# Kernel optimization log

Measured on AMD Instinct MI355X. Metric: run time of the kernel, lower is better.

Reference implementation:

```python
import jax, jax.numpy as jnp
import numpy as np

DIM = 768
N_HEADS = 12
HEAD_DIM = DIM // N_HEADS
MAX_REL = 3  # hardcoded in the module


def setup_inputs() -> dict:
    key = jax.random.key(0)
    ks = jax.random.split(key, 10)
    B, L = 4, 1024
    def xavier(k, shape):
        fan_in, fan_out = shape[-2], shape[-1]
        a = jnp.sqrt(6.0 / (fan_in + fan_out))
        return jax.random.uniform(k, shape, jnp.float32, -a, a)
    return {
        "query": jax.random.normal(ks[0], (B, L, DIM), jnp.float32),
        "key":   jax.random.normal(ks[1], (B, L, DIM), jnp.float32),
        "value": jax.random.normal(ks[2], (B, L, DIM), jnp.float32),
        "Wq": xavier(ks[3], (DIM, DIM)),
        "Wk": xavier(ks[4], (DIM, DIM)),
        "Wv": xavier(ks[5], (DIM, DIM)),
        "Wproj": xavier(ks[6], (DIM, DIM)),
        "b_proj": jnp.zeros((DIM,), jnp.float32),
        "rel_k_table": xavier(ks[7], (2 * MAX_REL + 1, HEAD_DIM)),
        "rel_v_table": xavier(ks[8], (2 * MAX_REL + 1, HEAD_DIM)),
    }


def _rel_embed(table, len_q, len_k):
    # [len_q, len_k, head_dim] gathered from clipped relative distances
    dist = jnp.arange(len_k)[None, :] - jnp.arange(len_q)[:, None]
    idx = jnp.clip(dist, -MAX_REL, MAX_REL) + MAX_REL
    return table[idx]


def reference(query, key, value, Wq, Wk, Wv, Wproj, b_proj, rel_k_table, rel_v_table):
    B, Lq, _ = query.shape
    Lk = key.shape[1]
    H, hd = N_HEADS, HEAD_DIM
    scale = hd ** (-0.5)

    q = query @ Wq.T                      # [B, Lq, D]
    k = key @ Wk.T                        # [B, Lk, D]
    v = value @ Wv.T                      # [B, Lk, D]

    qh = q.reshape(B, Lq, H, hd).transpose(0, 2, 1, 3)   # [B,H,Lq,hd]
    kh = k.reshape(B, Lk, H, hd).transpose(0, 2, 1, 3)
    vh = v.reshape(B, Lk, H, hd).transpose(0, 2, 1, 3)

    # content-content scores
    attn1 = jnp.einsum('bhqd,bhkd->bhqk', qh, kh)
    # content-relative-position scores
    rk = _rel_embed(rel_k_table, Lq, Lk)                  # [Lq,Lk,hd]
    attn2 = jnp.einsum('bhqd,qkd->bhqk', qh, rk)
    # NOTE: original code DIVIDES by scale (= hd**-0.5), i.e. multiplies by sqrt(hd)
    attn = (attn1 + attn2) / scale
    attn = jax.nn.softmax(attn, axis=-1)                  # [B,H,Lq,Lk]

    w1 = jnp.einsum('bhqk,bhkd->bhqd', attn, vh)
    rv = _rel_embed(rel_v_table, Lq, Lk)                  # [Lq,Lk,hd]
    w2 = jnp.einsum('bhqk,qkd->bhqd', attn, rv)

    x = (w1 + w2).transpose(0, 2, 1, 3).reshape(B, Lq, H * hd)
    x = x @ Wproj.T + b_proj
    return (x, attn)
```

## Files before the change

### kernel.cpp

```cpp
#include <hip/hip_runtime.h>

#define DIMM 768
#define NH 12
#define HD 64
#define LSEQ 1024
#define BATCH 4
#define NXE 3145728
#define NWE 589824

typedef __bf16 bf16x8 __attribute__((ext_vector_type(8)));
typedef float f32x4 __attribute__((ext_vector_type(4)));
typedef unsigned short u16;

static __device__ __forceinline__ u16 f2bf(float f) {
  unsigned u = __builtin_bit_cast(unsigned, f);
  u += 0x7fffu + ((u >> 16) & 1u);
  return (u16)(u >> 16);
}
static __device__ __forceinline__ float bf2f(u16 h) {
  unsigned u = ((unsigned)h) << 16;
  return __builtin_bit_cast(float, u);
}
static __device__ __forceinline__ bf16x8 ld8bf(const u16* p) {
  uint4 u = *(const uint4*)p;
  return __builtin_bit_cast(bf16x8, u);
}
#define MFMA(a, b, c) __builtin_amdgcn_mfma_f32_16x16x32_bf16(a, b, c, 0, 0, 0)
#define LGKM0_FENCE()                                      \
  do {                                                     \
    asm volatile("s_waitcnt lgkmcnt(0)" ::: "memory");     \
    __builtin_amdgcn_sched_barrier(0);                     \
    __builtin_amdgcn_s_barrier();                          \
  } while (0)

__global__ __launch_bounds__(256) void convert(
    const float* __restrict__ q_in, const float* __restrict__ k_in,
    const float* __restrict__ v_in, const float* __restrict__ Wq,
    const float* __restrict__ Wk, const float* __restrict__ Wv,
    const float* __restrict__ Wp, u16* __restrict__ AqH, u16* __restrict__ AqL,
    u16* __restrict__ AkH, u16* __restrict__ AkL, u16* __restrict__ Av,
    u16* __restrict__ WqH, u16* __restrict__ WqL, u16* __restrict__ WkH,
    u16* __restrict__ WkL, u16* __restrict__ Wvr, u16* __restrict__ Wpr) {
  long i = ((long)blockIdx.x * 256 + threadIdx.x) * 4;
  const float* src;
  u16 *dh, *dl = nullptr;
  long off;
  if (i < NXE) { src = q_in; dh = AqH; dl = AqL; off = i; }
  else if (i < 2L * NXE) { src = k_in; dh = AkH; dl = AkL; off = i - NXE; }
  else if (i < 3L * NXE) { src = v_in; dh = Av; off = i - 2L * NXE; }
  else {
    long j = i - 3L * NXE;
    int which = (int)(j / NWE);
    off = j % NWE;
    if (which == 0) { src = Wq; dh = WqH; dl = WqL; }
    else if (which == 1) { src = Wk; dh = WkH; dl = WkL; }
    else if (which == 2) { src = Wv; dh = Wvr; }
    else { src = Wp; dh = Wpr; }
  }
  float4 v = *(const float4*)(src + off);
  ushort4 h;
  h.x = f2bf(v.x); h.y = f2bf(v.y); h.z = f2bf(v.z); h.w = f2bf(v.w);
  *(ushort4*)(dh + off) = h;
  if (dl) {
    ushort4 lo;
    lo.x = f2bf(v.x - bf2f(h.x)); lo.y = f2bf(v.y - bf2f(h.y));
    lo.z = f2bf(v.z - bf2f(h.z)); lo.w = f2bf(v.w - bf2f(h.w));
    *(ushort4*)(dl + off) = lo;
  }
}

__device__ __forceinline__ void gemm_body(
    int mode, const u16* AqH, const u16* AqL, const u16* AkH, const u16* AkL,
    const u16* Av, const u16* WqH, const u16* WqL, const u16* WkH,
    const u16* WkL, const u16* Wvr, const u16* Wpr, const u16* wbuf,
    u16* qhi, u16* qlo, u16* khi, u16* klo, u16* vT, float* outp,
    const float* bias) {
  __shared__ u16 sAh[2][64 * 32], sAl[2][64 * 32];
  __shared__ u16 sBh[2][128 * 32], sBl[2][128 * 32];
  const u16 *Ah, *Al = nullptr, *Bh, *Bl = nullptr;
  if (mode == 0) { Ah = AqH; Al = AqL; Bh = WqH; Bl = WqL; }
  else if (mode == 1) { Ah = AkH; Al = AkL; Bh = WkH; Bl = WkL; }
  else if (mode == 2) { Ah = Av; Bh = Wvr; }
  else { Ah = wbuf; Bh = Wpr; }
  const int t = threadIdx.x, w = t >> 6, l = t & 63;
  const int quad = l >> 4, l15 = l & 15;
  const int flat = blockIdx.x + 64 * blockIdx.y;
  const int swz = (flat & 7) * 48 + (flat >> 3);
  const int m0 = (swz & 63) * 64, n0 = (swz >> 6) * 128;
  const int wm = (w & 1) * 32, wn = (w >> 1) * 64;
  const int srow = t >> 2, scol = (t & 3) * 8;
  const int t8 = t * 8;
  const u16* gA = Ah + (m0 + srow) * DIMM + scol;
  const u16* gB = Bh + (n0 + srow) * DIMM + scol;
  const u16* gAl = (mode < 2) ? Al + (m0 + srow) * DIMM + scol : nullptr;
  const u16* gBl = (mode < 2) ? Bl + (n0 + srow) * DIMM + scol : nullptr;
  f32x4 acc[2][4] = {};
  uint4 rA, rB0, rB1, rAl, rBl0, rBl1;

  if (mode < 2) {
#define LOADS2(k0n)                                                  \
    do {                                                             \
      rA = *(const uint4*)(gA + (k0n));                              \
      rB0 = *(const uint4*)(gB + (k0n));                             \
      rB1 = *(const uint4*)(gB + 64 * DIMM + (k0n));                 \
      rAl = *(const uint4*)(gAl + (k0n));                            \
      rBl0 = *(const uint4*)(gBl + (k0n));                           \
      rBl1 = *(const uint4*)(gBl + 64 * DIMM + (k0n));               \
    } while (0)
#define DSW2(p)                                                      \
    do {                                                             \
      *(uint4*)(&sAh[p][t8]) = rA;                                   \
      *(uint4*)(&sBh[p][t8]) = rB0;                                  \
      *(uint4*)(&sBh[p][t8 + 2048]) = rB1;                           \
      *(uint4*)(&sAl[p][t8]) = rAl;                                  \
      *(uint4*)(&sBl[p][t8]) = rBl0;                                 \
      *(uint4*)(&sBl[p][t8 + 2048]) = rBl1;                          \
    } while (0)
#define FRAGS2(p)                                                    \
    do {                                                             \
      _Pragma("unroll") for (int i = 0; i < 2; ++i) {                \
        ah[i] = __builtin_bit_cast(bf16x8,                           \
            *(const uint4*)(&sAh[p][(wm + i * 16 + l15) * 32 + quad * 8])); \
        al[i] = __builtin_bit_cast(bf16x8,                           \
            *(const uint4*)(&sAl[p][(wm + i * 16 + l15) * 32 + quad * 8])); \
      }                                                              \
      _Pragma("unroll") for (int j = 0; j < 4; ++j) {                \
        bh[j] = __builtin_bit_cast(bf16x8,                           \
            *(const uint4*)(&sBh[p][(wn + j * 16 + l15) * 32 + quad * 8])); \
        bl[j] = __builtin_bit_cast(bf16x8,                           \
            *(const uint4*)(&sBl[p][(wn + j * 16 + l15) * 32 + quad * 8])); \
      }                                                              \
    } while (0)
#define MFMAS2()                                                     \
    do {                                                             \
      _Pragma("unroll") for (int i = 0; i < 2; ++i)                  \
        _Pragma("unroll") for (int j = 0; j < 4; ++j)                \
          acc[i][j] = MFMA(ah[i], bh[j], acc[i][j]);                 \
      _Pragma("unroll") for (int i = 0; i < 2; ++i)                  \
        _Pragma("unroll") for (int j = 0; j < 4; ++j)                \
          acc[i][j] = MFMA(al[i], bh[j], acc[i][j]);                 \
      _Pragma("unroll") for (int i = 0; i < 2; ++i)                  \
        _Pragma("unroll") for (int j = 0; j < 4; ++j)                \
          acc[i][j] = MFMA(ah[i], bl[j], acc[i][j]);                 \
    } while (0)
    LOADS2(0);
    DSW2(0);
    LOADS2(32);
    LGKM0_FENCE();
    for (int k0 = 0; k0 < DIMM; k0 += 64) {
      bf16x8 ah[2], al[2], bh[4], bl[4];
      FRAGS2(0);
      DSW2(1);
      if (k0 + 64 < DIMM) LOADS2(k0 + 64);
      MFMAS2();
      LGKM0_FENCE();
      FRAGS2(1);
      if (k0 + 64 < DIMM) {
        DSW2(0);
        if (k0 + 96 < DIMM) LOADS2(k0 + 96);
      }
      MFMAS2();
      if (k0 + 64 < DIMM) LGKM0_FENCE();
    }
#undef LOADS2
#undef DSW2
#undef FRAGS2
#undef MFMAS2
  } else {
#define LOADS1(k0n)                                                  \
    do {                                                             \
      rA = *(const uint4*)(gA + (k0n));                              \
      rB0 = *(const uint4*)(gB + (k0n));                             \
      rB1 = *(const uint4*)(gB + 64 * DIMM + (k0n));                 \
    } while (0)
#define DSW1(p)                                                      \
    do {                                                             \
      *(uint4*)(&sAh[p][t8]) = rA;                                   \
      *(uint4*)(&sBh[p][t8]) = rB0;                                  \
      *(uint4*)(&sBh[p][t8 + 2048]) = rB1;                           \
    } while (0)
#define FRAGS1(p)                                                    \
    do {                                                             \
      _Pragma("unroll") for (int i = 0; i < 2; ++i)                  \
        ah[i] = __builtin_bit_cast(bf16x8,                           \
            *(const uint4*)(&sAh[p][(wm + i * 16 + l15) * 32 + quad * 8])); \
      _Pragma("unroll") for (int j = 0; j < 4; ++j)                  \
        bh[j] = __builtin_bit_cast(bf16x8,                           \
            *(const uint4*)(&sBh[p][(wn + j * 16 + l15) * 32 + quad * 8])); \
    } while (0)
#define MFMAS1()                                                     \
    do {                                                             \
      _Pragma("unroll") for (int i = 0; i < 2; ++i)                  \
        _Pragma("unroll") for (int j = 0; j < 4; ++j)                \
          acc[i][j] = MFMA(ah[i], bh[j], acc[i][j]);                 \
    } while (0)
    LOADS1(0);
    DSW1(0);
    LOADS1(32);
    LGKM0_FENCE();
    for (int k0 = 0; k0 < DIMM; k0 += 64) {
      bf16x8 ah[2], bh[4];
      FRAGS1(0);
      DSW1(1);
      if (k0 + 64 < DIMM) LOADS1(k0 + 64);
      MFMAS1();
      LGKM0_FENCE();
      FRAGS1(1);
      if (k0 + 64 < DIMM) {
        DSW1(0);
        if (k0 + 96 < DIMM) LOADS1(k0 + 96);
      }
      MFMAS1();
      if (k0 + 64 < DIMM) LGKM0_FENCE();
    }
#undef LOADS1
#undef DSW1
#undef FRAGS1
#undef MFMAS1
  }

  u16* oh = (mode == 0) ? qhi : khi;
  u16* ol = (mode == 0) ? qlo : klo;
#pragma unroll
  for (int i = 0; i < 2; ++i)
#pragma unroll
    for (int j = 0; j < 4; ++j)
#pragma unroll
      for (int r = 0; r < 4; ++r) {
        int grow = m0 + wm + i * 16 + quad * 4 + r;
        int gcol = n0 + wn + j * 16 + l15;
        float c = acc[i][j][r];
        int b = grow >> 10, ll = grow & 1023, h = gcol >> 6, d = gcol & 63;
        if (mode < 2) {
          int idx = ((b * NH + h) * LSEQ + ll) * HD + d;
          u16 hi = f2bf(c);
          oh[idx] = hi;
          ol[idx] = f2bf(c - bf2f(hi));
        } else if (mode == 2) {
          vT[((b * NH + h) * HD + d) * LSEQ + ll] = f2bf(c);
        } else {
          outp[grow * DIMM + gcol] = c + bias[gcol];
        }
      }
}

__global__ __launch_bounds__(256, 3) void gemm_qkv(
    const u16* __restrict__ AqH, const u16* __restrict__ AqL,
    const u16* __restrict__ AkH, const u16* __restrict__ AkL,
    const u16* __restrict__ Av, const u16* __restrict__ WqH,
    const u16* __restrict__ WqL, const u16* __restrict__ WkH,
    const u16* __restrict__ WkL, const u16* __restrict__ Wvr,
    const u16* __restrict__ Wpr, const u16* __restrict__ wbuf,
    u16* __restrict__ qhi, u16* __restrict__ qlo, u16* __restrict__ khi,
    u16* __restrict__ klo, u16* __restrict__ vT, float* __restrict__ outp,
    const float* __restrict__ bias) {
  gemm_body(blockIdx.z, AqH, AqL, AkH, AkL, Av, WqH, WqL, WkH, WkL, Wvr, Wpr,
            wbuf, qhi, qlo, khi, klo, vT, outp, bias);
}

__global__ __launch_bounds__(256, 3) void gemm_proj(
    const u16* __restrict__ AqH, const u16* __restrict__ AqL,
    const u16* __restrict__ AkH, const u16* __restrict__ AkL,
    const u16* __restrict__ Av, const u16* __restrict__ WqH,
    const u16* __restrict__ WqL, const u16* __restrict__ WkH,
    const u16* __restrict__ WkL, const u16* __restrict__ Wvr,
    const u16* __restrict__ Wpr, const u16* __restrict__ wbuf,
    u16* __restrict__ qhi, u16* __restrict__ qlo, u16* __restrict__ khi,
    u16* __restrict__ klo, u16* __restrict__ vT, float* __restrict__ outp,
    const float* __restrict__ bias) {
  gemm_body(3, AqH, AqL, AkH, AkL, Av, WqH, WqL, WkH, WkL, Wvr, Wpr,
            wbuf, qhi, qlo, khi, klo, vT, outp, bias);
}

__global__ __launch_bounds__(256, 3) void attn_core(
    const u16* __restrict__ qhi, const u16* __restrict__ qlo,
    const u16* __restrict__ khi, const u16* __restrict__ klo,
    const u16* __restrict__ vT, const float* __restrict__ relk,
    const float* __restrict__ relv, float* __restrict__ attn_out,
    u16* __restrict__ wbuf) {
  __shared__ __align__(16) u16 uni[16 * 1032];
  __shared__ float qrel[16][7];
  __shared__ float arel[16][7];
  __shared__ float rvt[7][64];
  __shared__ float red[4][16][4];

  const int Lb = blockIdx.x + 64 * (blockIdx.y + NH * blockIdx.z);
  const int flat = (Lb & 7) * 384 + (Lb >> 3);
  const int qt = flat & 63, h = (flat >> 6) % NH, b = flat / (64 * NH);
  const int q0 = qt * 16;
  const int tid = threadIdx.x, wave = tid >> 6, lane = tid & 63;
  const int quad = lane >> 4, l15 = lane & 15;
  const int bhd = b * NH + h;

  const int rs = tid >> 3;
  const int cg = (tid & 7) ^ (rs & 7);
  const u16* gh = khi + (bhd * LSEQ + rs) * HD + cg * 8;
  const u16* gl = klo + (bhd * LSEQ + rs) * HD + cg * 8;
  u16* const wslot = uni + tid * 8;
  const int rowA = wave * 16 + l15;
  const int sw = rowA & 7;
  const int s0 = (rowA * 8 + (quad ^ sw)) * 8;
  const int s1 = (rowA * 8 + ((quad + 4) ^ sw)) * 8;

  uint4 sA0, sA1, sA2, sA3, sB0, sB1, sB2, sB3;
#define LOADA(c)                                                     \
  do {                                                               \
    sA0 = *(const uint4*)(gh + (c) * (64 * HD));                     \
    sA1 = *(const uint4*)(gh + (c) * (64 * HD) + 32 * HD);           \
    sA2 = *(const uint4*)(gl + (c) * (64 * HD));                     \
    sA3 = *(const uint4*)(gl + (c) * (64 * HD) + 32 * HD);           \
  } while (0)
#define LOADB(c)                                                     \
  do {                                                               \
    sB0 = *(const uint4*)(gh + (c) * (64 * HD));                     \
    sB1 = *(const uint4*)(gh + (c) * (64 * HD) + 32 * HD);           \
    sB2 = *(const uint4*)(gl + (c) * (64 * HD));                     \
    sB3 = *(const uint4*)(gl + (c) * (64 * HD) + 32 * HD);           \
  } while (0)
#define DSWRITE_A(bufsel)                                            \
  do {                                                               \
    u16* d_ = wslot + (bufsel) * 8192;                               \
    *(uint4*)(d_) = sA0;                                             \
    *(uint4*)(d_ + 2048) = sA1;                                      \
    *(uint4*)(d_ + 4096) = sA2;                                      \
    *(uint4*)(d_ + 6144) = sA3;                                      \
  } while (0)
#define DSWRITE_B(bufsel)                                            \
  do {                                                               \
    u16* d_ = wslot + (bufsel) * 8192;                               \
    *(uint4*)(d_) = sB0;                                             \
    *(uint4*)(d_ + 2048) = sB1;                                      \
    *(uint4*)(d_ + 4096) = sB2;                                      \
    *(uint4*)(d_ + 6144) = sB3;                                      \
  } while (0)

  const int qbase = (bhd * LSEQ + q0 + l15) * HD + quad * 8;
  bf16x8 ah0 = ld8bf(qhi + qbase);
  bf16x8 ah1 = ld8bf(qhi + qbase + 32);
  bf16x8 al0 = ld8bf(qlo + qbase);
  bf16x8 al1 = ld8bf(qlo + qbase + 32);
  LOADA(0);
  LOADB(1);

  for (int t = tid; t < 7 * HD; t += 256) rvt[t >> 6][t & 63] = relv[t];
  if (tid < 112) {
    int q = tid / 7, rr = tid % 7;
    const u16* qp = qhi + (bhd * LSEQ + q0 + q) * HD;
    const u16* lp = qlo + (bhd * LSEQ + q0 + q) * HD;
    const float* tp = relk + rr * HD;
    float s = 0.f;
#pragma unroll
    for (int d8 = 0; d8 < HD; d8 += 8) {
      uint4 uh = *(const uint4*)(qp + d8);
      uint4 ul = *(const uint4*)(lp + d8);
      float4 t0 = *(const float4*)(tp + d8);
      float4 t1 = *(const float4*)(tp + d8 + 4);
      unsigned hh[4] = {uh.x, uh.y, uh.z, uh.w};
      unsigned lv[4] = {ul.x, ul.y, ul.z, ul.w};
      float tv[8] = {t0.x, t0.y, t0.z, t0.w, t1.x, t1.y, t1.z, t1.w};
#pragma unroll
      for (int m = 0; m < 4; ++m) {
        s += (bf2f((u16)(hh[m] & 0xffff)) + bf2f((u16)(lv[m] & 0xffff))) * tv[2 * m];
        s += (bf2f((u16)(hh[m] >> 16)) + bf2f((u16)(lv[m] >> 16))) * tv[2 * m + 1];
      }
    }
    qrel[q][rr] = s;
    arel[q][rr] = 0.f;
  }

  DSWRITE_A(0);
  asm volatile("s_waitcnt lgkmcnt(0)" ::: "memory");
  __builtin_amdgcn_sched_barrier(0);
  __builtin_amdgcn_s_barrier();

  f32x4 sc[16];
#pragma unroll
  for (int c = 0; c < 16; ++c) {
    const u16* cur = uni + (c & 1) * 8192;
    bf16x8 kh0 = ld8bf(cur + s0);
    bf16x8 kh1 = ld8bf(cur + s1);
    bf16x8 kl0 = ld8bf(cur + 4096 + s0);
    bf16x8 kl1 = ld8bf(cur + 4096 + s1);
    f32x4 e = {}, f = {};
    e = MFMA(ah0, kh0, e);
    f = MFMA(ah1, kh1, f);
    e = MFMA(ah0, kl0, e);
    f = MFMA(ah1, kl1, f);
    e = MFMA(al0, kh0, e);
    f = MFMA(al1, kh1, f);
    sc[c] = e + f;
    if (c < 14) {
      if ((c & 1) == 0) LOADA(c + 2); else LOADB(c + 2);
    }
    if (c < 15) {
      if ((c & 1) == 0) DSWRITE_B(1); else DSWRITE_A(0);
      asm volatile("s_waitcnt lgkmcnt(0)" ::: "memory");
      __builtin_amdgcn_sched_barrier(0);
      __builtin_amdgcn_s_barrier();
    }
  }
#undef LOADA
#undef LOADB
#undef DSWRITE_A
#undef DSWRITE_B

  const int colbase = wave * 16 + l15;
  const int dbase = colbase - q0 - quad * 4;
  float mrow[4] = {-3.4e38f, -3.4e38f, -3.4e38f, -3.4e38f};
#pragma unroll
  for (int c = 0; c < 16; ++c)
#pragma unroll
    for (int r = 0; r < 4; ++r) {
      int d = dbase + c * 64 - r;
      int ri = d < -3 ? 0 : (d > 3 ? 6 : d + 3);
      float s = (sc[c][r] + qrel[quad * 4 + r][ri]) * 8.0f;
      sc[c][r] = s;
      mrow[r] = fmaxf(mrow[r], s);
    }
#pragma unroll
  for (int m = 1; m <= 8; m <<= 1)
#pragma unroll
    for (int r = 0; r < 4; ++r) mrow[r] = fmaxf(mrow[r], __shfl_xor(mrow[r], m));
  if (l15 < 4) {
    float mv = l15 == 0 ? mrow[0] : l15 == 1 ? mrow[1] : l15 == 2 ? mrow[2] : mrow[3];
    red[0][quad * 4 + l15][wave] = mv;
  }
  __syncthreads();
  float mx[4];
#pragma unroll
  for (int r = 0; r < 4; ++r) {
    int row = quad * 4 + r;
    mx[r] = fmaxf(fmaxf(red[0][row][0], red[0][row][1]),
                  fmaxf(red[0][row][2], red[0][row][3]));
  }

  float sum[4] = {}, s0a[4] = {}, s6a[4] = {};
#pragma unroll
  for (int c = 0; c < 16; ++c)
#pragma unroll
    for (int r = 0; r < 4; ++r) {
      float e = __expf(sc[c][r] - mx[r]);
      sc[c][r] = e;
      int d = dbase + c * 64 - r;
      sum[r] += e;
      if (d <= -3) s0a[r] += e;
      if (d >= 3) s6a[r] += e;
    }
#pragma unroll
  for (int m = 1; m <= 8; m <<= 1)
#pragma unroll
    for (int r = 0; r < 4; ++r) {
      sum[r] += __shfl_xor(sum[r], m);
      s0a[r] += __shfl_xor(s0a[r], m);
      s6a[r] += __shfl_xor(s6a[r], m);
    }
  if (l15 < 4) {
    int row = quad * 4 + l15;
    float sv = l15 == 0 ? sum[0] : l15 == 1 ? sum[1] : l15 == 2 ? sum[2] : sum[3];
    float a0 = l15 == 0 ? s0a[0] : l15 == 1 ? s0a[1] : l15 == 2 ? s0a[2] : s0a[3];
    float a6 = l15 == 0 ? s6a[0] : l15 == 1 ? s6a[1] : l15 == 2 ? s6a[2] : s6a[3];
    red[1][row][wave] = sv;
    red[2][row][wave] = a0;
    red[3][row][wave] = a6;
  }
  __syncthreads();
  float rn[4];
#pragma unroll
  for (int r = 0; r < 4; ++r) {
    int row = quad * 4 + r;
    float s = red[1][row][0] + red[1][row][1] + red[1][row][2] + red[1][row][3];
    rn[r] = 1.0f / s;
    if (wave == 0 && l15 == 0) {
      float t0 = red[2][row][0] + red[2][row][1] + red[2][row][2] + red[2][row][3];
      float t6 = red[3][row][0] + red[3][row][1] + red[3][row][2] + red[3][row][3];
      arel[row][0] = t0 * rn[r];
      arel[row][6] = t6 * rn[r];
    }
  }

#pragma unroll
  for (int c = 0; c < 16; ++c) {
    int col = colbase + c * 64;
#pragma unroll
    for (int r = 0; r < 4; ++r) {
      int row = quad * 4 + r;
      float p = sc[c][r] * rn[r];
      uni[row * 1032 + col] = f2bf(p);
      int d = dbase + c * 64 - r;
      if (d >= -2 && d <= 2) arel[row][d + 3] = p;
    }
  }
  __syncthreads();

  {
    float* aob = attn_out + ((size_t)(bhd * LSEQ + q0)) * LSEQ;
#pragma unroll
    for (int row = 0; row < 16; ++row) {
      uint2 u = *(const uint2*)&uni[row * 1032 + tid * 4];
      float4 f = {bf2f((u16)(u.x & 0xffff)), bf2f((u16)(u.x >> 16)),
                  bf2f((u16)(u.y & 0xffff)), bf2f((u16)(u.y >> 16))};
      *(float4*)(aob + row * LSEQ + tid * 4) = f;
    }
  }

  {
    const u16* vb = vT + (bhd * HD + wave * 16 + l15) * LSEQ;
    f32x4 acc0 = {}, acc1 = {};
#pragma unroll 4
    for (int kk = 0; kk < LSEQ; kk += 64) {
      int ak = kk + quad * 8;
      bf16x8 aP0 = __builtin_bit_cast(bf16x8, *(const uint4*)&uni[l15 * 1032 + ak]);
      bf16x8 bV0 = ld8bf(vb + ak);
      acc0 = MFMA(aP0, bV0, acc0);
      bf16x8 aP1 = __builtin_bit_cast(bf16x8, *(const uint4*)&uni[l15 * 1032 + ak + 32]);
      bf16x8 bV1 = ld8bf(vb + ak + 32);
      acc1 = MFMA(aP1, bV1, acc1);
    }
    f32x4 acc = acc0 + acc1;
    const int col = wave * 16 + l15;
#pragma unroll
    for (int r = 0; r < 4; ++r) {
      int row = quad * 4 + r;
      float w2 = 0.f;
#pragma unroll
      for (int t = 0; t < 7; ++t) w2 += arel[row][t] * rvt[t][col];
      wbuf[(b * LSEQ + q0 + row) * DIMM + h * HD + col] = f2bf(acc[r] + w2);
    }
  }
}

extern "C" void kernel_launch(void* const* d_in, const int* in_sizes, int n_in,
                              void* d_out, int out_size, void* d_ws, size_t ws_size,
                              hipStream_t stream) {
  const float* q_in = (const float*)d_in[0];
  const float* k_in = (const float*)d_in[1];
  const float* v_in = (const float*)d_in[2];
  const float* Wq = (const float*)d_in[3];
  const float* Wk = (const float*)d_in[4];
  const float* Wv = (const float*)d_in[5];
  const float* Wp = (const float*)d_in[6];
  const float* bias = (const float*)d_in[7];
  const float* relk = (const float*)d_in[8];
  const float* relv = (const float*)d_in[9];
  float* out = (float*)d_out;

  u16* p = (u16*)d_ws;
  u16 *AqH = p, *AqL = AqH + NXE, *AkH = AqL + NXE, *AkL = AkH + NXE,
      *Av = AkL + NXE;
  u16 *WqH = Av + NXE, *WqL = WqH + NWE, *WkH = WqL + NWE, *WkL = WkH + NWE,
      *Wvr = WkL + NWE, *Wpr = Wvr + NWE;
  u16 *qhi = Wpr + NWE, *qlo = qhi + NXE, *khi = qlo + NXE, *klo = khi + NXE,
      *vT = klo + NXE, *wbuf = vT + NXE;

  convert<<<(3 * NXE + 4 * NWE) / 1024, 256, 0, stream>>>(
      q_in, k_in, v_in, Wq, Wk, Wv, Wp, AqH, AqL, AkH, AkL, Av, WqH, WqL, WkH,
      WkL, Wvr, Wpr);
  gemm_qkv<<<dim3(64, 6, 3), 256, 0, stream>>>(
      AqH, AqL, AkH, AkL, Av, WqH, WqL, WkH, WkL, Wvr, Wpr, wbuf, qhi, qlo,
      khi, klo, vT, out, bias);
  attn_core<<<dim3(64, NH, BATCH), 256, 0, stream>>>(
      qhi, qlo, khi, klo, vT, relk, relv, out + NXE, wbuf);
  gemm_proj<<<dim3(64, 6, 1), 256, 0, stream>>>(
      AqH, AqL, AkH, AkL, Av, WqH, WqL, WkH, WkL, Wvr, Wpr, wbuf, qhi, qlo,
      khi, klo, vT, out, bias);
}
```

Before: 426.6 us.

## Load K fragments directly from global memory instead of LDS double-buffering

```diff
diff --git a/kernel.cpp b/kernel.cpp
--- a/kernel.cpp
+++ b/kernel.cpp
@@ -292,55 +292,11 @@
   const int quad = lane >> 4, l15 = lane & 15;
   const int bhd = b * NH + h;
 
-  const int rs = tid >> 3;
-  const int cg = (tid & 7) ^ (rs & 7);
-  const u16* gh = khi + (bhd * LSEQ + rs) * HD + cg * 8;
-  const u16* gl = klo + (bhd * LSEQ + rs) * HD + cg * 8;
-  u16* const wslot = uni + tid * 8;
-  const int rowA = wave * 16 + l15;
-  const int sw = rowA & 7;
-  const int s0 = (rowA * 8 + (quad ^ sw)) * 8;
-  const int s1 = (rowA * 8 + ((quad + 4) ^ sw)) * 8;
-
-  uint4 sA0, sA1, sA2, sA3, sB0, sB1, sB2, sB3;
-#define LOADA(c)                                                     \
-  do {                                                               \
-    sA0 = *(const uint4*)(gh + (c) * (64 * HD));                     \
-    sA1 = *(const uint4*)(gh + (c) * (64 * HD) + 32 * HD);           \
-    sA2 = *(const uint4*)(gl + (c) * (64 * HD));                     \
-    sA3 = *(const uint4*)(gl + (c) * (64 * HD) + 32 * HD);           \
-  } while (0)
-#define LOADB(c)                                                     \
-  do {                                                               \
-    sB0 = *(const uint4*)(gh + (c) * (64 * HD));                     \
-    sB1 = *(const uint4*)(gh + (c) * (64 * HD) + 32 * HD);           \
-    sB2 = *(const uint4*)(gl + (c) * (64 * HD));                     \
-    sB3 = *(const uint4*)(gl + (c) * (64 * HD) + 32 * HD);           \
-  } while (0)
-#define DSWRITE_A(bufsel)                                            \
-  do {                                                               \
-    u16* d_ = wslot + (bufsel) * 8192;                               \
-    *(uint4*)(d_) = sA0;                                             \
-    *(uint4*)(d_ + 2048) = sA1;                                      \
-    *(uint4*)(d_ + 4096) = sA2;                                      \
-    *(uint4*)(d_ + 6144) = sA3;                                      \
-  } while (0)
-#define DSWRITE_B(bufsel)                                            \
-  do {                                                               \
-    u16* d_ = wslot + (bufsel) * 8192;                               \
-    *(uint4*)(d_) = sB0;                                             \
-    *(uint4*)(d_ + 2048) = sB1;                                      \
-    *(uint4*)(d_ + 4096) = sB2;                                      \
-    *(uint4*)(d_ + 6144) = sB3;                                      \
-  } while (0)
-
   const int qbase = (bhd * LSEQ + q0 + l15) * HD + quad * 8;
   bf16x8 ah0 = ld8bf(qhi + qbase);
   bf16x8 ah1 = ld8bf(qhi + qbase + 32);
   bf16x8 al0 = ld8bf(qlo + qbase);
   bf16x8 al1 = ld8bf(qlo + qbase + 32);
-  LOADA(0);
-  LOADB(1);
 
   for (int t = tid; t < 7 * HD; t += 256) rvt[t >> 6][t & 63] = relv[t];
   if (tid < 112) {
@@ -368,41 +324,29 @@
     arel[q][rr] = 0.f;
   }
 
-  DSWRITE_A(0);
-  asm volatile("s_waitcnt lgkmcnt(0)" ::: "memory");
-  __builtin_amdgcn_sched_barrier(0);
-  __builtin_amdgcn_s_barrier();
-
   f32x4 sc[16];
-#pragma unroll
-  for (int c = 0; c < 16; ++c) {
-    const u16* cur = uni + (c & 1) * 8192;
-    bf16x8 kh0 = ld8bf(cur + s0);
-    bf16x8 kh1 = ld8bf(cur + s1);
-    bf16x8 kl0 = ld8bf(cur + 4096 + s0);
-    bf16x8 kl1 = ld8bf(cur + 4096 + s1);
-    f32x4 e = {}, f = {};
-    e = MFMA(ah0, kh0, e);
-    f = MFMA(ah1, kh1, f);
-    e = MFMA(ah0, kl0, e);
-    f = MFMA(ah1, kl1, f);
-    e = MFMA(al0, kh0, e);
-    f = MFMA(al1, kh1, f);
-    sc[c] = e + f;
-    if (c < 14) {
-      if ((c & 1) == 0) LOADA(c + 2); else LOADB(c + 2);
-    }
-    if (c < 15) {
-      if ((c & 1) == 0) DSWRITE_B(1); else DSWRITE_A(0);
-      asm volatile("s_waitcnt lgkmcnt(0)" ::: "memory");
-      __builtin_amdgcn_sched_barrier(0);
-      __builtin_amdgcn_s_barrier();
-    }
-  }
-#undef LOADA
-#undef LOADB
-#undef DSWRITE_A
-#undef DSWRITE_B
+  {
+    const u16* gh = khi + (bhd * LSEQ + wave * 16 + l15) * HD + quad * 8;
+    const u16* gl = klo + (bhd * LSEQ + wave * 16 + l15) * HD + quad * 8;
+#pragma unroll 4
+    for (int c = 0; c < 16; ++c) {
+      const u16* ph = gh + c * (64 * HD);
+      const u16* pl = gl + c * (64 * HD);
+      bf16x8 kh0 = ld8bf(ph);
+      bf16x8 kh1 = ld8bf(ph + 32);
+      bf16x8 kl0 = ld8bf(pl);
+      bf16x8 kl1 = ld8bf(pl + 32);
+      f32x4 e = {}, f = {};
+      e = MFMA(ah0, kh0, e);
+      f = MFMA(ah1, kh1, f);
+      e = MFMA(ah0, kl0, e);
+      f = MFMA(ah1, kl1, f);
+      e = MFMA(al0, kh0, e);
+      f = MFMA(al1, kh1, f);
+      sc[c] = e + f;
+    }
+  }
+  __syncthreads();
 
   const int colbase = wave * 16 + l15;
   const int dbase = colbase - q0 - quad * 4;
```

New measurement: 584.5 us. 1.37x slower.
